# Performance work log

Hardware: AMD Instinct MI355X
Metric: run time of the kernel (lower is better)

## Reference

```python
import jax, jax.numpy as jnp
import numpy as np

N_NODES = 100000
N_EDGES = 3200000
IN_FEATS = 768
HIDDEN = 32
NUM_CLASSES = 8


def setup_inputs() -> dict:
    key = jax.random.key(0)
    ks = jax.random.split(key, 9)
    feats = jax.random.normal(ks[0], (N_NODES, IN_FEATS), dtype=jnp.float32)
    src = jax.random.randint(ks[1], (N_EDGES,), 0, N_NODES, dtype=jnp.int32)
    dst = jax.random.randint(ks[2], (N_EDGES,), 0, N_NODES, dtype=jnp.int32)
    # DGL SAGEConv params: fc_self / fc_neigh (bias=False) + separate bias
    def glorot(k, shape):
        lim = float(np.sqrt(6.0 / (shape[0] + shape[1])))
        return jax.random.uniform(k, shape, jnp.float32, -lim, lim)
    W_self1 = glorot(ks[3], (HIDDEN, IN_FEATS))
    W_neigh1 = glorot(ks[4], (HIDDEN, IN_FEATS))
    b1 = jnp.zeros((HIDDEN,), jnp.float32)
    W_self2 = glorot(ks[5], (NUM_CLASSES, HIDDEN))
    W_neigh2 = glorot(ks[6], (NUM_CLASSES, HIDDEN))
    b2 = jnp.zeros((NUM_CLASSES,), jnp.float32)
    return {"features": feats, "src": src, "dst": dst,
            "W_self1": W_self1, "W_neigh1": W_neigh1, "b1": b1,
            "W_self2": W_self2, "W_neigh2": W_neigh2, "b2": b2}


def _sage_mean_layer(x, W_self, W_neigh, b, src, dst, n_nodes):
    # DGL: lin_before_mp when in_feats > out_feats (true for both layers here)
    h = x @ W_neigh.T                      # [N, out]
    msg = h[src]                           # [E, out] gather
    agg_sum = jax.ops.segment_sum(msg, dst, num_segments=n_nodes)
    deg = jax.ops.segment_sum(jnp.ones_like(dst, dtype=x.dtype), dst,
                              num_segments=n_nodes)
    h_neigh = agg_sum / jnp.maximum(deg, 1.0)[:, None]  # zero-in-degree -> 0
    return x @ W_self.T + h_neigh + b


def reference(features, src, dst, W_self1, W_neigh1, b1, W_self2, W_neigh2, b2):
    n = features.shape[0]
    h = _sage_mean_layer(features, W_self1, W_neigh1, b1, src, dst, n)
    h = jax.nn.relu(h)
    # dropout is identity in eval mode
    out = _sage_mean_layer(h, W_self2, W_neigh2, b2, src, dst, n)
    return out
```

## Files before the change

kernel.cpp:

```cpp
#include <hip/hip_runtime.h>
#include <hip/hip_bf16.h>

#define IN_FEATS 768
#define PART_CHUNK 8192
#define SRC_BITS 17
#define SRC_MASK 0x1FFFF

typedef __attribute__((ext_vector_type(8))) short short8v;
typedef __attribute__((ext_vector_type(4))) float f32x4;

__device__ __forceinline__ unsigned short f2bf(float f) {
    union { float f; unsigned int u; } c; c.f = f;
    unsigned int r = (c.u + 0x7FFFu + ((c.u >> 16) & 1u)) >> 16;
    return (unsigned short)r;
}
__device__ __forceinline__ float bflo(unsigned int v) {
    union { unsigned int u; float f; } c; c.u = v << 16; return c.f;
}
__device__ __forceinline__ float bfhi(unsigned int v) {
    union { unsigned int u; float f; } c; c.u = v & 0xFFFF0000u; return c.f;
}
__device__ __forceinline__ short8v pack8(float4 p, float4 q) {
    short8v r;
    r[0] = (short)f2bf(p.x); r[1] = (short)f2bf(p.y);
    r[2] = (short)f2bf(p.z); r[3] = (short)f2bf(p.w);
    r[4] = (short)f2bf(q.x); r[5] = (short)f2bf(q.y);
    r[6] = (short)f2bf(q.z); r[7] = (short)f2bf(q.w);
    return r;
}

__global__ __launch_bounds__(512) void init_cursor_kernel(
    int* __restrict__ bcursor, int NB, int CAP)
{
    const int t = threadIdx.x;
    if (t < NB) bcursor[t] = t * CAP;
}

__global__ __launch_bounds__(256) void gemm_part_kernel(
    const float* __restrict__ x,
    const float* __restrict__ Wn,
    const float* __restrict__ Ws,
    const float* __restrict__ b1,
    unsigned short* __restrict__ hn1b,
    float* __restrict__ hs1,
    int N,
    const int* __restrict__ src, const int* __restrict__ dst,
    int* __restrict__ bcursor, unsigned int* __restrict__ packed,
    int NB, int E, int CAP, int nbPart)
{
    __shared__ __align__(16) unsigned char smem[36864];
    const int tid = threadIdx.x;

    if ((int)blockIdx.x < nbPart) {
        int* hcnt  = (int*)smem;
        int* hbase = hcnt + 512;

        for (int i = tid; i < NB; i += 256) hcnt[i] = 0;
        __syncthreads();

        const int start = blockIdx.x * PART_CHUNK;
        const int end   = min(start + PART_CHUNK, E);
        const int vend  = start + ((end - start) & ~3);

        for (int i = start + tid * 4; i + 3 < end; i += 1024) {
            const int4 d4 = *(const int4*)&dst[i];
            atomicAdd(&hcnt[d4.x >> 8], 1);
            atomicAdd(&hcnt[d4.y >> 8], 1);
            atomicAdd(&hcnt[d4.z >> 8], 1);
            atomicAdd(&hcnt[d4.w >> 8], 1);
        }
        for (int i = vend + tid; i < end; i += 256)
            atomicAdd(&hcnt[dst[i] >> 8], 1);
        __syncthreads();

        for (int i = tid; i < NB; i += 256) {
            const int c = hcnt[i];
            hbase[i] = c ? atomicAdd(&bcursor[i], c) : 0;
            hcnt[i] = 0;
        }
        __syncthreads();

        for (int i = start + tid * 4; i + 3 < end; i += 1024) {
            const int4 d4 = *(const int4*)&dst[i];
            const int4 s4 = *(const int4*)&src[i];
            {
                const int b = d4.x >> 8;
                const int p = hbase[b] + atomicAdd(&hcnt[b], 1);
                if (p < (b + 1) * CAP) packed[p] = ((unsigned int)(d4.x & 255) << SRC_BITS) | (unsigned int)s4.x;
            }
            {
                const int b = d4.y >> 8;
                const int p = hbase[b] + atomicAdd(&hcnt[b], 1);
                if (p < (b + 1) * CAP) packed[p] = ((unsigned int)(d4.y & 255) << SRC_BITS) | (unsigned int)s4.y;
            }
            {
                const int b = d4.z >> 8;
                const int p = hbase[b] + atomicAdd(&hcnt[b], 1);
                if (p < (b + 1) * CAP) packed[p] = ((unsigned int)(d4.z & 255) << SRC_BITS) | (unsigned int)s4.z;
            }
            {
                const int b = d4.w >> 8;
                const int p = hbase[b] + atomicAdd(&hcnt[b], 1);
                if (p < (b + 1) * CAP) packed[p] = ((unsigned int)(d4.w & 255) << SRC_BITS) | (unsigned int)s4.w;
            }
        }
        for (int i = vend + tid; i < end; i += 256) {
            const int d = dst[i];
            const int b = d >> 8;
            const int p = hbase[b] + atomicAdd(&hcnt[b], 1);
            if (p < (b + 1) * CAP) packed[p] = ((unsigned int)(d & 255) << SRC_BITS) | (unsigned int)src[i];
        }
        return;
    }

    unsigned short* AsB = (unsigned short*)smem;
    unsigned short* BsB = AsB + 2 * 64 * 72;
#define AS(b, r) (AsB + ((b) * 64 + (r)) * 72)
#define BS(b, r) (BsB + ((b) * 64 + (r)) * 72)

    const int lrow = tid >> 2;
    const int lk16 = (tid & 3) * 16;
    const int row0 = ((int)blockIdx.x - nbPart) * 64;

    const int  grow   = row0 + lrow;
    const bool rvalid = (grow < N);
    const float* xrow = x + (size_t)(rvalid ? grow : (N - 1)) * IN_FEATS;
    const float* wrow = (lrow < 32) ? (Wn + (size_t)lrow * IN_FEATS)
                                    : (Ws + (size_t)(lrow - 32) * IN_FEATS);

    const int w    = tid >> 6;
    const int l    = tid & 63;
    const int lr16 = l & 15;
    const int lk   = (l >> 4) * 8;

    f32x4 acc[4];
#pragma unroll
    for (int ct = 0; ct < 4; ++ct) acc[ct] = (f32x4){0.f, 0.f, 0.f, 0.f};

    float4 a0, a1, a2, a3, w0, w1, w2, w3;
    a0 = *(const float4*)(xrow + lk16 + 0);
    a1 = *(const float4*)(xrow + lk16 + 4);
    a2 = *(const float4*)(xrow + lk16 + 8);
    a3 = *(const float4*)(xrow + lk16 + 12);
    w0 = *(const float4*)(wrow + lk16 + 0);
    w1 = *(const float4*)(wrow + lk16 + 4);
    w2 = *(const float4*)(wrow + lk16 + 8);
    w3 = *(const float4*)(wrow + lk16 + 12);

    const int NSTEP = IN_FEATS / 64;
    for (int step = 0; step < NSTEP; ++step) {
        const int buf = step & 1;
        *(short8v*)(AS(buf, lrow) + lk16)     = pack8(a0, a1);
        *(short8v*)(AS(buf, lrow) + lk16 + 8) = pack8(a2, a3);
        *(short8v*)(BS(buf, lrow) + lk16)     = pack8(w0, w1);
        *(short8v*)(BS(buf, lrow) + lk16 + 8) = pack8(w2, w3);
        __syncthreads();

        if (step + 1 < NSTEP) {
            const int k0 = (step + 1) * 64;
            a0 = *(const float4*)(xrow + k0 + lk16 + 0);
            a1 = *(const float4*)(xrow + k0 + lk16 + 4);
            a2 = *(const float4*)(xrow + k0 + lk16 + 8);
            a3 = *(const float4*)(xrow + k0 + lk16 + 12);
            w0 = *(const float4*)(wrow + k0 + lk16 + 0);
            w1 = *(const float4*)(wrow + k0 + lk16 + 4);
            w2 = *(const float4*)(wrow + k0 + lk16 + 8);
            w3 = *(const float4*)(wrow + k0 + lk16 + 12);
        }

        short8v af0 = *(const short8v*)(AS(buf, w * 16 + lr16) + lk);
        short8v af1 = *(const short8v*)(AS(buf, w * 16 + lr16) + lk + 32);
#pragma unroll
        for (int ct = 0; ct < 4; ++ct) {
            short8v bf0 = *(const short8v*)(BS(buf, ct * 16 + lr16) + lk);
            acc[ct] = __builtin_amdgcn_mfma_f32_16x16x32_bf16(af0, bf0, acc[ct], 0, 0, 0);
        }
#pragma unroll
        for (int ct = 0; ct < 4; ++ct) {
            short8v bf1 = *(const short8v*)(BS(buf, ct * 16 + lr16) + lk + 32);
            acc[ct] = __builtin_amdgcn_mfma_f32_16x16x32_bf16(af1, bf1, acc[ct], 0, 0, 0);
        }
    }
#undef AS
#undef BS

    const int rbase = row0 + w * 16 + (l >> 4) * 4;
#pragma unroll
    for (int ct = 0; ct < 4; ++ct) {
        const int ncol = ct * 16 + lr16;
        if (ncol < 32) {
            const int half = ncol >> 4;
            const int c16  = ncol & 15;
            unsigned short* hd = hn1b + (size_t)half * N * 16;
#pragma unroll
            for (int j = 0; j < 4; ++j) {
                const int r = rbase + j;
                if (r < N) hd[(size_t)r * 16 + c16] = f2bf(acc[ct][j]);
            }
        } else {
            const int c = ncol - 32;
            const float bias = b1[c];
#pragma unroll
            for (int j = 0; j < 4; ++j) {
                const int r = rbase + j;
                if (r < N) hs1[(size_t)r * 32 + c] = acc[ct][j] + bias;
            }
        }
    }
}

__global__ __launch_bounds__(1024) void csr_finalize_kernel(
    const unsigned int* __restrict__ packed, const int* __restrict__ bcursor,
    int* __restrict__ rowstart, int* __restrict__ rowcnt,
    int* __restrict__ edge_src, int N, int CAP)
{
    __shared__ int cnt[256];
    __shared__ int sdata[256];
    __shared__ int cur[256];
    const int b = blockIdx.x;
    const int t = threadIdx.x;
    const int base = b * CAP;
    const int endp = min(bcursor[b], base + CAP);

    if (t < 256) cnt[t] = 0;
    __syncthreads();
    for (int i = base + t; i < endp; i += 1024)
        atomicAdd(&cnt[packed[i] >> SRC_BITS], 1);
    __syncthreads();

    if (t < 256) sdata[t] = cnt[t];
    __syncthreads();
    for (int off = 1; off < 256; off <<= 1) {
        const int add = (t < 256 && t >= off) ? sdata[t - off] : 0;
        __syncthreads();
        if (t < 256) sdata[t] += add;
        __syncthreads();
    }
    if (t < 256) {
        const int excl = (t > 0) ? sdata[t - 1] : 0;
        const int n = (b << 8) + t;
        if (n < N) {
            rowstart[n] = base + excl;
            rowcnt[n]   = cnt[t];
        }
        cur[t] = base + excl;
    }
    __syncthreads();

    for (int i = base + t; i < endp; i += 1024) {
        const unsigned int v = packed[i];
        const int pos = atomicAdd(&cur[v >> SRC_BITS], 1);
        edge_src[pos] = (int)(v & SRC_MASK);
    }
}

__global__ __launch_bounds__(256) void agg1_fused_kernel(
    const unsigned short* __restrict__ hn1b,
    const float* __restrict__ hs1,
    const int* __restrict__ rowstart, const int* __restrict__ rowcnt,
    const int* __restrict__ edge_src,
    const float* __restrict__ Wn2, const float* __restrict__ Ws2,
    const float* __restrict__ b2,
    unsigned short* __restrict__ hn2b, float* __restrict__ hs2, int N)
{
    __shared__ float w2[16][33];
    __shared__ float bb[8];
    __shared__ float hsm[32][33];

    const int tid = threadIdx.x;
    const int g   = tid >> 3;
    const int ln  = tid & 7;

    w2[tid >> 5][tid & 31]       = Wn2[tid];
    w2[8 + (tid >> 5)][tid & 31] = Ws2[tid];
    if (tid < 8) bb[tid] = b2[tid];

    const int n = blockIdx.x * 32 + g;
    int rs = 0, degi = 0;
    if (n < N) { rs = rowstart[n]; degi = rowcnt[n]; }
    const float inv = 1.0f / fmaxf((float)degi, 1.0f);
    const int re = rs + degi;

#pragma unroll
    for (int h = 0; h < 2; ++h) {
        const unsigned int* tab = (const unsigned int*)hn1b + (size_t)h * N * 8;
        float sx = 0.f, sy = 0.f;
        if (n < N) {
            int e = rs;
            for (; e + 4 <= re; e += 4) {
                const int s0 = edge_src[e + 0];
                const int s1 = edge_src[e + 1];
                const int s2 = edge_src[e + 2];
                const int s3 = edge_src[e + 3];
                const unsigned int v0 = tab[(size_t)s0 * 8 + ln];
                const unsigned int v1 = tab[(size_t)s1 * 8 + ln];
                const unsigned int v2 = tab[(size_t)s2 * 8 + ln];
                const unsigned int v3 = tab[(size_t)s3 * 8 + ln];
                sx += (bflo(v0) + bflo(v1)) + (bflo(v2) + bflo(v3));
                sy += (bfhi(v0) + bfhi(v1)) + (bfhi(v2) + bfhi(v3));
            }
            for (; e < re; ++e) {
                const unsigned int v = tab[(size_t)edge_src[e] * 8 + ln];
                sx += bflo(v); sy += bfhi(v);
            }
            const int f = h * 16 + 2 * ln;
            const float2 hsv = *(const float2*)(hs1 + (size_t)n * 32 + f);
            hsm[g][f + 0] = fmaxf(hsv.x + sx * inv, 0.0f);
            hsm[g][f + 1] = fmaxf(hsv.y + sy * inv, 0.0f);
        }
    }
    __syncthreads();

    if (n < N) {
        const float* hv = hsm[g];
#pragma unroll
        for (int o2 = 0; o2 < 2; ++o2) {
            const int o = o2 * 8 + ln;
            const float* wr = w2[o];
            float acc = 0.0f;
#pragma unroll
            for (int k = 0; k < 32; ++k) acc += wr[k] * hv[k];
            if (o < 8) hn2b[(size_t)n * 8 + o] = f2bf(acc);
            else       hs2[(size_t)n * 8 + (o - 8)] = acc + bb[o - 8];
        }
    }
}

__global__ __launch_bounds__(256) void agg2_fused_kernel(
    const unsigned short* __restrict__ hn2b, const float* __restrict__ hs2,
    const int* __restrict__ rowstart, const int* __restrict__ rowcnt,
    const int* __restrict__ edge_src,
    float* __restrict__ out, int N)
{
    const int tid  = threadIdx.x;
    const int g    = tid >> 4;
    const int ln   = tid & 15;
    const int slot = ln >> 2;
    const int q    = ln & 3;

    const unsigned int* hn2u = (const unsigned int*)hn2b;

    const int n = blockIdx.x * 16 + g;
    float sx = 0.f, sy = 0.f;
    int degi = 0;
    if (n < N) {
        const int rs = rowstart[n];
        degi = rowcnt[n];
        const int re = rs + degi;
        for (int e = rs + slot; e < re; e += 4) {
            const unsigned int v = hn2u[(size_t)edge_src[e] * 4 + q];
            sx += bflo(v); sy += bfhi(v);
        }
    }
    sx += __shfl_xor(sx, 4, 64);  sy += __shfl_xor(sy, 4, 64);
    sx += __shfl_xor(sx, 8, 64);  sy += __shfl_xor(sy, 8, 64);

    if (n < N && slot == 0) {
        const float inv = 1.0f / fmaxf((float)degi, 1.0f);
        const float2 s = *(const float2*)(hs2 + (size_t)n * 8 + 2 * q);
        float2 o;
        o.x = s.x + sx * inv;
        o.y = s.y + sy * inv;
        *(float2*)(out + (size_t)n * 8 + 2 * q) = o;
    }
}

extern "C" void kernel_launch(void* const* d_in, const int* in_sizes, int n_in,
                              void* d_out, int out_size, void* d_ws, size_t ws_size,
                              hipStream_t stream)
{
    const float* feats = (const float*)d_in[0];
    const int*   src   = (const int*)d_in[1];
    const int*   dst   = (const int*)d_in[2];
    const float* Ws1   = (const float*)d_in[3];
    const float* Wn1   = (const float*)d_in[4];
    const float* b1    = (const float*)d_in[5];
    const float* Ws2   = (const float*)d_in[6];
    const float* Wn2   = (const float*)d_in[7];
    const float* b2    = (const float*)d_in[8];
    float* out = (float*)d_out;

    const int N  = in_sizes[0] / IN_FEATS;
    const int E  = in_sizes[1];
    const int NB = (N + 255) >> 8;
    const int CAP = (int)((((2LL * E) / NB) + 255) & ~255LL);

    char* ws = (char*)d_ws;
    const size_t N32 = (size_t)N * 32;
    const size_t N8  = (size_t)N * 8;
    unsigned short* hn1b = (unsigned short*)ws;
    ws += ((N32 * 2 + 255) / 256) * 256;
    float* hs1 = (float*)ws;
    ws += ((N32 * 4 + 255) / 256) * 256;
    unsigned short* hn2b = (unsigned short*)ws;
    ws += ((N8 * 2 + 255) / 256) * 256;
    float* hs2 = (float*)ws;
    ws += ((N8 * 4 + 255) / 256) * 256;
    int* rowstart = (int*)ws;
    ws += (((size_t)N * 4 + 255) / 256) * 256;
    int* rowcnt = (int*)ws;
    ws += (((size_t)N * 4 + 255) / 256) * 256;
    int* bcursor = (int*)ws;
    ws += 512 * 4;
    unsigned int* packed = (unsigned int*)ws;
    ws += (((size_t)NB * CAP * 4 + 255) / 256) * 256;
    int* edge_src = (int*)ws;

    const int nbPart = (E + PART_CHUNK - 1) / PART_CHUNK;
    const int nbGemm = (N + 63) / 64;

    init_cursor_kernel<<<1, 512, 0, stream>>>(bcursor, NB, CAP);

    gemm_part_kernel<<<nbPart + nbGemm, 256, 0, stream>>>(
        feats, Wn1, Ws1, b1, hn1b, hs1, N,
        src, dst, bcursor, packed, NB, E, CAP, nbPart);

    csr_finalize_kernel<<<NB, 1024, 0, stream>>>(packed, bcursor, rowstart,
                                                 rowcnt, edge_src, N, CAP);

    agg1_fused_kernel<<<(N + 31) / 32, 256, 0, stream>>>(
        hn1b, hs1, rowstart, rowcnt, edge_src, Wn2, Ws2, b2, hn2b, hs2, N);

    agg2_fused_kernel<<<(N + 15) / 16, 256, 0, stream>>>(
        hn2b, hs2, rowstart, rowcnt, edge_src, out, N);
}
```

Baseline: 239.3 us.

## Merge all stages into one persistent cooperative kernel with grid syncs

Replaces five separate kernel launches (cursor init, partition+GEMM, CSR finalize, layer-1 aggregation, layer-2 aggregation) with a single cooperative persistent kernel that loops over work items and uses grid-wide syncs between stages. The aim is to remove launch gaps and the tail effects at kernel boundaries. In exchange the grid is capped at 4 blocks per CU times 256 CUs, which may lower occupancy for the memory-bound gather phases. The finalize stage also drops from 1024 to 256 threads per bucket, and grid.sync adds barrier overhead.

```diff
diff --git a/kernel.cpp b/kernel.cpp
--- a/kernel.cpp
+++ b/kernel.cpp
@@ -1,5 +1,8 @@
 #include <hip/hip_runtime.h>
+#include <hip/hip_cooperative_groups.h>
 #include <hip/hip_bf16.h>
+
+namespace cg = cooperative_groups;
 
 #define IN_FEATS 768
 #define PART_CHUNK 8192
@@ -29,104 +32,107 @@
     return r;
 }
 
-__global__ __launch_bounds__(512) void init_cursor_kernel(
-    int* __restrict__ bcursor, int NB, int CAP)
+struct MegaParams {
+    const float* x;
+    const float* Wn;
+    const float* Ws;
+    const float* b1;
+    const float* Wn2;
+    const float* Ws2;
+    const float* b2;
+    const int* src;
+    const int* dst;
+    unsigned short* hn1b;
+    float* hs1;
+    unsigned short* hn2b;
+    float* hs2;
+    int* rowstart;
+    int* rowcnt;
+    int* bcursor;
+    unsigned int* packed;
+    int* edge_src;
+    float* out;
+    int N, E, NB, CAP, nbPart, nbGemm;
+};
+
+__device__ __forceinline__ void partition_chunk(
+    const MegaParams& p, int chunk, int tid, unsigned char* smem)
 {
-    const int t = threadIdx.x;
-    if (t < NB) bcursor[t] = t * CAP;
-}
-
-__global__ __launch_bounds__(256) void gemm_part_kernel(
-    const float* __restrict__ x,
-    const float* __restrict__ Wn,
-    const float* __restrict__ Ws,
-    const float* __restrict__ b1,
-    unsigned short* __restrict__ hn1b,
-    float* __restrict__ hs1,
-    int N,
-    const int* __restrict__ src, const int* __restrict__ dst,
-    int* __restrict__ bcursor, unsigned int* __restrict__ packed,
-    int NB, int E, int CAP, int nbPart)
+    int* hcnt  = (int*)smem;
+    int* hbase = hcnt + 512;
+
+    for (int i = tid; i < p.NB; i += 256) hcnt[i] = 0;
+    __syncthreads();
+
+    const int start = chunk * PART_CHUNK;
+    const int end   = min(start + PART_CHUNK, p.E);
+    const int vend  = start + ((end - start) & ~3);
+
+    for (int i = start + tid * 4; i + 3 < end; i += 1024) {
+        const int4 d4 = *(const int4*)&p.dst[i];
+        atomicAdd(&hcnt[d4.x >> 8], 1);
+        atomicAdd(&hcnt[d4.y >> 8], 1);
+        atomicAdd(&hcnt[d4.z >> 8], 1);
+        atomicAdd(&hcnt[d4.w >> 8], 1);
+    }
+    for (int i = vend + tid; i < end; i += 256)
+        atomicAdd(&hcnt[p.dst[i] >> 8], 1);
+    __syncthreads();
+
+    for (int i = tid; i < p.NB; i += 256) {
+        const int c = hcnt[i];
+        hbase[i] = c ? atomicAdd(&p.bcursor[i], c) : 0;
+        hcnt[i] = 0;
+    }
+    __syncthreads();
+
+    for (int i = start + tid * 4; i + 3 < end; i += 1024) {
+        const int4 d4 = *(const int4*)&p.dst[i];
+        const int4 s4 = *(const int4*)&p.src[i];
+        {
+            const int b = d4.x >> 8;
+            const int q = hbase[b] + atomicAdd(&hcnt[b], 1);
+            if (q < (b + 1) * p.CAP) p.packed[q] = ((unsigned int)(d4.x & 255) << SRC_BITS) | (unsigned int)s4.x;
+        }
+        {
+            const int b = d4.y >> 8;
+            const int q = hbase[b] + atomicAdd(&hcnt[b], 1);
+            if (q < (b + 1) * p.CAP) p.packed[q] = ((unsigned int)(d4.y & 255) << SRC_BITS) | (unsigned int)s4.y;
+        }
+        {
+            const int b = d4.z >> 8;
+            const int q = hbase[b] + atomicAdd(&hcnt[b], 1);
+            if (q < (b + 1) * p.CAP) p.packed[q] = ((unsigned int)(d4.z & 255) << SRC_BITS) | (unsigned int)s4.z;
+        }
+        {
+            const int b = d4.w >> 8;
+            const int q = hbase[b] + atomicAdd(&hcnt[b], 1);
+            if (q < (b + 1) * p.CAP) p.packed[q] = ((unsigned int)(d4.w & 255) << SRC_BITS) | (unsigned int)s4.w;
+        }
+    }
+    for (int i = vend + tid; i < end; i += 256) {
+        const int d = p.dst[i];
+        const int b = d >> 8;
+        const int q = hbase[b] + atomicAdd(&hcnt[b], 1);
+        if (q < (b + 1) * p.CAP) p.packed[q] = ((unsigned int)(d & 255) << SRC_BITS) | (unsigned int)p.src[i];
+    }
+}
+
+__device__ __forceinline__ void gemm_tile(
+    const MegaParams& p, int t, int tid, unsigned char* smem)
 {
-    __shared__ __align__(16) unsigned char smem[36864];
-    const int tid = threadIdx.x;
-
-    if ((int)blockIdx.x < nbPart) {
-        int* hcnt  = (int*)smem;
-        int* hbase = hcnt + 512;
-
-        for (int i = tid; i < NB; i += 256) hcnt[i] = 0;
-        __syncthreads();
-
-        const int start = blockIdx.x * PART_CHUNK;
-        const int end   = min(start + PART_CHUNK, E);
-        const int vend  = start + ((end - start) & ~3);
-
-        for (int i = start + tid * 4; i + 3 < end; i += 1024) {
-            const int4 d4 = *(const int4*)&dst[i];
-            atomicAdd(&hcnt[d4.x >> 8], 1);
-            atomicAdd(&hcnt[d4.y >> 8], 1);
-            atomicAdd(&hcnt[d4.z >> 8], 1);
-            atomicAdd(&hcnt[d4.w >> 8], 1);
-        }
-        for (int i = vend + tid; i < end; i += 256)
-            atomicAdd(&hcnt[dst[i] >> 8], 1);
-        __syncthreads();
-
-        for (int i = tid; i < NB; i += 256) {
-            const int c = hcnt[i];
-            hbase[i] = c ? atomicAdd(&bcursor[i], c) : 0;
-            hcnt[i] = 0;
-        }
-        __syncthreads();
-
-        for (int i = start + tid * 4; i + 3 < end; i += 1024) {
-            const int4 d4 = *(const int4*)&dst[i];
-            const int4 s4 = *(const int4*)&src[i];
-            {
-                const int b = d4.x >> 8;
-                const int p = hbase[b] + atomicAdd(&hcnt[b], 1);
-                if (p < (b + 1) * CAP) packed[p] = ((unsigned int)(d4.x & 255) << SRC_BITS) | (unsigned int)s4.x;
-            }
-            {
-                const int b = d4.y >> 8;
-                const int p = hbase[b] + atomicAdd(&hcnt[b], 1);
-                if (p < (b + 1) * CAP) packed[p] = ((unsigned int)(d4.y & 255) << SRC_BITS) | (unsigned int)s4.y;
-            }
-            {
-                const int b = d4.z >> 8;
-                const int p = hbase[b] + atomicAdd(&hcnt[b], 1);
-                if (p < (b + 1) * CAP) packed[p] = ((unsigned int)(d4.z & 255) << SRC_BITS) | (unsigned int)s4.z;
-            }
-            {
-                const int b = d4.w >> 8;
-                const int p = hbase[b] + atomicAdd(&hcnt[b], 1);
-                if (p < (b + 1) * CAP) packed[p] = ((unsigned int)(d4.w & 255) << SRC_BITS) | (unsigned int)s4.w;
-            }
-        }
-        for (int i = vend + tid; i < end; i += 256) {
-            const int d = dst[i];
-            const int b = d >> 8;
-            const int p = hbase[b] + atomicAdd(&hcnt[b], 1);
-            if (p < (b + 1) * CAP) packed[p] = ((unsigned int)(d & 255) << SRC_BITS) | (unsigned int)src[i];
-        }
-        return;
-    }
-
     unsigned short* AsB = (unsigned short*)smem;
     unsigned short* BsB = AsB + 2 * 64 * 72;
-#define AS(b, r) (AsB + ((b) * 64 + (r)) * 72)
-#define BS(b, r) (BsB + ((b) * 64 + (r)) * 72)
 
     const int lrow = tid >> 2;
     const int lk16 = (tid & 3) * 16;
-    const int row0 = ((int)blockIdx.x - nbPart) * 64;
+    const int row0 = t * 64;
 
     const int  grow   = row0 + lrow;
-    const bool rvalid = (grow < N);
-    const float* xrow = x + (size_t)(rvalid ? grow : (N - 1)) * IN_FEATS;
-    const float* wrow = (lrow < 32) ? (Wn + (size_t)lrow * IN_FEATS)
-                                    : (Ws + (size_t)(lrow - 32) * IN_FEATS);
+    const bool rvalid = (grow < p.N);
+    const float* xrow = p.x + (size_t)(rvalid ? grow : (p.N - 1)) * IN_FEATS;
+    const float* wrow = (lrow < 32) ? (p.Wn + (size_t)lrow * IN_FEATS)
+                                    : (p.Ws + (size_t)(lrow - 32) * IN_FEATS);
 
     const int w    = tid >> 6;
     const int l    = tid & 63;
@@ -150,10 +156,12 @@
     const int NSTEP = IN_FEATS / 64;
     for (int step = 0; step < NSTEP; ++step) {
         const int buf = step & 1;
-        *(short8v*)(AS(buf, lrow) + lk16)     = pack8(a0, a1);
-        *(short8v*)(AS(buf, lrow) + lk16 + 8) = pack8(a2, a3);
-        *(short8v*)(BS(buf, lrow) + lk16)     = pack8(w0, w1);
-        *(short8v*)(BS(buf, lrow) + lk16 + 8) = pack8(w2, w3);
+        unsigned short* as = AsB + (buf * 64 + lrow) * 72;
+        unsigned short* bs = BsB + (buf * 64 + lrow) * 72;
+        *(short8v*)(as + lk16)     = pack8(a0, a1);
+        *(short8v*)(as + lk16 + 8) = pack8(a2, a3);
+        *(short8v*)(bs + lk16)     = pack8(w0, w1);
+        *(short8v*)(bs + lk16 + 8) = pack8(w2, w3);
         __syncthreads();
 
         if (step + 1 < NSTEP) {
@@ -168,21 +176,22 @@
             w3 = *(const float4*)(wrow + k0 + lk16 + 12);
         }
 
-        short8v af0 = *(const short8v*)(AS(buf, w * 16 + lr16) + lk);
-        short8v af1 = *(const short8v*)(AS(buf, w * 16 + lr16) + lk + 32);
+        const unsigned short* ar = AsB + (buf * 64 + w * 16 + lr16) * 72;
+        short8v af0 = *(const short8v*)(ar + lk);
+        short8v af1 = *(const short8v*)(ar + lk + 32);
 #pragma unroll
         for (int ct = 0; ct < 4; ++ct) {
-            short8v bf0 = *(const short8v*)(BS(buf, ct * 16 + lr16) + lk);
+            const unsigned short* br = BsB + (buf * 64 + ct * 16 + lr16) * 72;
+            short8v bf0 = *(const short8v*)(br + lk);
             acc[ct] = __builtin_amdgcn_mfma_f32_16x16x32_bf16(af0, bf0, acc[ct], 0, 0, 0);
         }
 #pragma unroll
         for (int ct = 0; ct < 4; ++ct) {
-            short8v bf1 = *(const short8v*)(BS(buf, ct * 16 + lr16) + lk + 32);
+            const unsigned short* br = BsB + (buf * 64 + ct * 16 + lr16) * 72;
+            short8v bf1 = *(const short8v*)(br + lk + 32);
             acc[ct] = __builtin_amdgcn_mfma_f32_16x16x32_bf16(af1, bf1, acc[ct], 0, 0, 0);
         }
     }
-#undef AS
-#undef BS
 
     const int rbase = row0 + w * 16 + (l >> 4) * 4;
 #pragma unroll
@@ -191,177 +200,192 @@
         if (ncol < 32) {
             const int half = ncol >> 4;
             const int c16  = ncol & 15;
-            unsigned short* hd = hn1b + (size_t)half * N * 16;
+            unsigned short* hd = p.hn1b + (size_t)half * p.N * 16;
 #pragma unroll
             for (int j = 0; j < 4; ++j) {
                 const int r = rbase + j;
-                if (r < N) hd[(size_t)r * 16 + c16] = f2bf(acc[ct][j]);
+                if (r < p.N) hd[(size_t)r * 16 + c16] = f2bf(acc[ct][j]);
             }
         } else {
             const int c = ncol - 32;
-            const float bias = b1[c];
+            const float bias = p.b1[c];
 #pragma unroll
             for (int j = 0; j < 4; ++j) {
                 const int r = rbase + j;
-                if (r < N) hs1[(size_t)r * 32 + c] = acc[ct][j] + bias;
-            }
-        }
-    }
-}
-
-__global__ __launch_bounds__(1024) void csr_finalize_kernel(
-    const unsigned int* __restrict__ packed, const int* __restrict__ bcursor,
-    int* __restrict__ rowstart, int* __restrict__ rowcnt,
-    int* __restrict__ edge_src, int N, int CAP)
+                if (r < p.N) p.hs1[(size_t)r * 32 + c] = acc[ct][j] + bias;
+            }
+        }
+    }
+}
+
+__device__ __forceinline__ void finalize_bucket(
+    const MegaParams& p, int b, int tid, unsigned char* smem)
 {
-    __shared__ int cnt[256];
-    __shared__ int sdata[256];
-    __shared__ int cur[256];
-    const int b = blockIdx.x;
-    const int t = threadIdx.x;
-    const int base = b * CAP;
-    const int endp = min(bcursor[b], base + CAP);
-
-    if (t < 256) cnt[t] = 0;
-    __syncthreads();
-    for (int i = base + t; i < endp; i += 1024)
-        atomicAdd(&cnt[packed[i] >> SRC_BITS], 1);
-    __syncthreads();
-
-    if (t < 256) sdata[t] = cnt[t];
+    int* cnt   = (int*)smem;
+    int* sdata = cnt + 256;
+    int* cur   = sdata + 256;
+
+    const int base = b * p.CAP;
+    const int endp = min(p.bcursor[b], base + p.CAP);
+
+    cnt[tid] = 0;
+    __syncthreads();
+    for (int i = base + tid; i < endp; i += 256)
+        atomicAdd(&cnt[p.packed[i] >> SRC_BITS], 1);
+    __syncthreads();
+
+    sdata[tid] = cnt[tid];
     __syncthreads();
     for (int off = 1; off < 256; off <<= 1) {
-        const int add = (t < 256 && t >= off) ? sdata[t - off] : 0;
-        __syncthreads();
-        if (t < 256) sdata[t] += add;
-        __syncthreads();
-    }
-    if (t < 256) {
-        const int excl = (t > 0) ? sdata[t - 1] : 0;
-        const int n = (b << 8) + t;
-        if (n < N) {
-            rowstart[n] = base + excl;
-            rowcnt[n]   = cnt[t];
-        }
-        cur[t] = base + excl;
-    }
-    __syncthreads();
-
-    for (int i = base + t; i < endp; i += 1024) {
-        const unsigned int v = packed[i];
+        const int add = (tid >= off) ? sdata[tid - off] : 0;
+        __syncthreads();
+        sdata[tid] += add;
+        __syncthreads();
+    }
+    const int excl = (tid > 0) ? sdata[tid - 1] : 0;
+    const int n = (b << 8) + tid;
+    if (n < p.N) {
+        p.rowstart[n] = base + excl;
+        p.rowcnt[n]   = cnt[tid];
+    }
+    cur[tid] = base + excl;
+    __syncthreads();
+
+    for (int i = base + tid; i < endp; i += 256) {
+        const unsigned int v = p.packed[i];
         const int pos = atomicAdd(&cur[v >> SRC_BITS], 1);
-        edge_src[pos] = (int)(v & SRC_MASK);
-    }
-}
-
-__global__ __launch_bounds__(256) void agg1_fused_kernel(
-    const unsigned short* __restrict__ hn1b,
-    const float* __restrict__ hs1,
-    const int* __restrict__ rowstart, const int* __restrict__ rowcnt,
-    const int* __restrict__ edge_src,
-    const float* __restrict__ Wn2, const float* __restrict__ Ws2,
-    const float* __restrict__ b2,
-    unsigned short* __restrict__ hn2b, float* __restrict__ hs2, int N)
+        p.edge_src[pos] = (int)(v & SRC_MASK);
+    }
+}
+
+__global__ __launch_bounds__(256, 4) void mega_kernel(MegaParams p)
 {
-    __shared__ float w2[16][33];
-    __shared__ float bb[8];
-    __shared__ float hsm[32][33];
-
-    const int tid = threadIdx.x;
-    const int g   = tid >> 3;
-    const int ln  = tid & 7;
-
-    w2[tid >> 5][tid & 31]       = Wn2[tid];
-    w2[8 + (tid >> 5)][tid & 31] = Ws2[tid];
-    if (tid < 8) bb[tid] = b2[tid];
-
-    const int n = blockIdx.x * 32 + g;
-    int rs = 0, degi = 0;
-    if (n < N) { rs = rowstart[n]; degi = rowcnt[n]; }
-    const float inv = 1.0f / fmaxf((float)degi, 1.0f);
-    const int re = rs + degi;
-
-#pragma unroll
-    for (int h = 0; h < 2; ++h) {
-        const unsigned int* tab = (const unsigned int*)hn1b + (size_t)h * N * 8;
-        float sx = 0.f, sy = 0.f;
-        if (n < N) {
-            int e = rs;
-            for (; e + 4 <= re; e += 4) {
-                const int s0 = edge_src[e + 0];
-                const int s1 = edge_src[e + 1];
-                const int s2 = edge_src[e + 2];
-                const int s3 = edge_src[e + 3];
-                const unsigned int v0 = tab[(size_t)s0 * 8 + ln];
-                const unsigned int v1 = tab[(size_t)s1 * 8 + ln];
-                const unsigned int v2 = tab[(size_t)s2 * 8 + ln];
-                const unsigned int v3 = tab[(size_t)s3 * 8 + ln];
-                sx += (bflo(v0) + bflo(v1)) + (bflo(v2) + bflo(v3));
-                sy += (bfhi(v0) + bfhi(v1)) + (bfhi(v2) + bfhi(v3));
-            }
-            for (; e < re; ++e) {
-                const unsigned int v = tab[(size_t)edge_src[e] * 8 + ln];
-                sx += bflo(v); sy += bfhi(v);
-            }
-            const int f = h * 16 + 2 * ln;
-            const float2 hsv = *(const float2*)(hs1 + (size_t)n * 32 + f);
-            hsm[g][f + 0] = fmaxf(hsv.x + sx * inv, 0.0f);
-            hsm[g][f + 1] = fmaxf(hsv.y + sy * inv, 0.0f);
-        }
-    }
-    __syncthreads();
-
-    if (n < N) {
-        const float* hv = hsm[g];
-#pragma unroll
-        for (int o2 = 0; o2 < 2; ++o2) {
-            const int o = o2 * 8 + ln;
-            const float* wr = w2[o];
-            float acc = 0.0f;
-#pragma unroll
-            for (int k = 0; k < 32; ++k) acc += wr[k] * hv[k];
-            if (o < 8) hn2b[(size_t)n * 8 + o] = f2bf(acc);
-            else       hs2[(size_t)n * 8 + (o - 8)] = acc + bb[o - 8];
-        }
-    }
-}
-
-__global__ __launch_bounds__(256) void agg2_fused_kernel(
-    const unsigned short* __restrict__ hn2b, const float* __restrict__ hs2,
-    const int* __restrict__ rowstart, const int* __restrict__ rowcnt,
-    const int* __restrict__ edge_src,
-    float* __restrict__ out, int N)
-{
+    __shared__ __align__(16) unsigned char smem[36864];
+    cg::grid_group gg = cg::this_grid();
     const int tid  = threadIdx.x;
-    const int g    = tid >> 4;
-    const int ln   = tid & 15;
-    const int slot = ln >> 2;
-    const int q    = ln & 3;
-
-    const unsigned int* hn2u = (const unsigned int*)hn2b;
-
-    const int n = blockIdx.x * 16 + g;
-    float sx = 0.f, sy = 0.f;
-    int degi = 0;
-    if (n < N) {
-        const int rs = rowstart[n];
-        degi = rowcnt[n];
-        const int re = rs + degi;
-        for (int e = rs + slot; e < re; e += 4) {
-            const unsigned int v = hn2u[(size_t)edge_src[e] * 4 + q];
-            sx += bflo(v); sy += bfhi(v);
-        }
-    }
-    sx += __shfl_xor(sx, 4, 64);  sy += __shfl_xor(sy, 4, 64);
-    sx += __shfl_xor(sx, 8, 64);  sy += __shfl_xor(sy, 8, 64);
-
-    if (n < N && slot == 0) {
-        const float inv = 1.0f / fmaxf((float)degi, 1.0f);
-        const float2 s = *(const float2*)(hs2 + (size_t)n * 8 + 2 * q);
-        float2 o;
-        o.x = s.x + sx * inv;
-        o.y = s.y + sy * inv;
-        *(float2*)(out + (size_t)n * 8 + 2 * q) = o;
+    const int bid  = blockIdx.x;
+    const int nblk = gridDim.x;
+
+    for (int i = bid * 256 + tid; i < p.NB; i += nblk * 256)
+        p.bcursor[i] = i * p.CAP;
+    gg.sync();
+
+    const int totalP1 = p.nbPart + p.nbGemm;
+    for (int item = bid; item < totalP1; item += nblk) {
+        if (item < p.nbPart) partition_chunk(p, item, tid, smem);
+        else                 gemm_tile(p, item - p.nbPart, tid, smem);
+        __syncthreads();
+    }
+    gg.sync();
+
+    for (int b = bid; b < p.NB; b += nblk) {
+        finalize_bucket(p, b, tid, smem);
+        __syncthreads();
+    }
+    gg.sync();
+
+    {
+        float* w2  = (float*)smem;
+        float* bb  = w2 + 16 * 33;
+        float* hsm = bb + 8;
+
+        w2[(tid >> 5) * 33 + (tid & 31)]       = p.Wn2[tid];
+        w2[(8 + (tid >> 5)) * 33 + (tid & 31)] = p.Ws2[tid];
+        if (tid < 8) bb[tid] = p.b2[tid];
+        __syncthreads();
+
+        const int g  = tid >> 3;
+        const int ln = tid & 7;
+        const int ngroups = (p.N + 31) / 32;
+
+        for (int gi = bid; gi < ngroups; gi += nblk) {
+            const int n = gi * 32 + g;
+            int rs = 0, degi = 0;
+            if (n < p.N) { rs = p.rowstart[n]; degi = p.rowcnt[n]; }
+            const float inv = 1.0f / fmaxf((float)degi, 1.0f);
+            const int re = rs + degi;
+
+#pragma unroll
+            for (int h = 0; h < 2; ++h) {
+                const unsigned int* tab = (const unsigned int*)p.hn1b + (size_t)h * p.N * 8;
+                float sx = 0.f, sy = 0.f;
+                if (n < p.N) {
+                    int e = rs;
+                    for (; e + 4 <= re; e += 4) {
+                        const int s0 = p.edge_src[e + 0];
+                        const int s1 = p.edge_src[e + 1];
+                        const int s2 = p.edge_src[e + 2];
+                        const int s3 = p.edge_src[e + 3];
+                        const unsigned int v0 = tab[(size_t)s0 * 8 + ln];
+                        const unsigned int v1 = tab[(size_t)s1 * 8 + ln];
+                        const unsigned int v2 = tab[(size_t)s2 * 8 + ln];
+                        const unsigned int v3 = tab[(size_t)s3 * 8 + ln];
+                        sx += (bflo(v0) + bflo(v1)) + (bflo(v2) + bflo(v3));
+                        sy += (bfhi(v0) + bfhi(v1)) + (bfhi(v2) + bfhi(v3));
+                    }
+                    for (; e < re; ++e) {
+                        const unsigned int v = tab[(size_t)p.edge_src[e] * 8 + ln];
+                        sx += bflo(v); sy += bfhi(v);
+                    }
+                    const int f = h * 16 + 2 * ln;
+                    const float2 hsv = *(const float2*)(p.hs1 + (size_t)n * 32 + f);
+                    hsm[g * 33 + f + 0] = fmaxf(hsv.x + sx * inv, 0.0f);
+                    hsm[g * 33 + f + 1] = fmaxf(hsv.y + sy * inv, 0.0f);
+                }
+            }
+            __syncthreads();
+
+            if (n < p.N) {
+                const float* hv = hsm + g * 33;
+#pragma unroll
+                for (int o2 = 0; o2 < 2; ++o2) {
+                    const int o = o2 * 8 + ln;
+                    const float* wr = w2 + o * 33;
+                    float acc = 0.0f;
+#pragma unroll
+                    for (int k = 0; k < 32; ++k) acc += wr[k] * hv[k];
+                    if (o < 8) p.hn2b[(size_t)n * 8 + o] = f2bf(acc);
+                    else       p.hs2[(size_t)n * 8 + (o - 8)] = acc + bb[o - 8];
+                }
+            }
+            __syncthreads();
+        }
+    }
+    gg.sync();
+
+    {
+        const int g    = tid >> 4;
+        const int ln   = tid & 15;
+        const int slot = ln >> 2;
+        const int q    = ln & 3;
+        const unsigned int* hn2u = (const unsigned int*)p.hn2b;
+        const int ng2 = (p.N + 15) / 16;
+
+        for (int gi = bid; gi < ng2; gi += nblk) {
+            const int n = gi * 16 + g;
+            float sx = 0.f, sy = 0.f;
+            int degi = 0;
+            if (n < p.N) {
+                const int rs = p.rowstart[n];
+                degi = p.rowcnt[n];
+                const int re = rs + degi;
+                for (int e = rs + slot; e < re; e += 4) {
+                    const unsigned int v = hn2u[(size_t)p.edge_src[e] * 4 + q];
+                    sx += bflo(v); sy += bfhi(v);
+                }
+            }
+            sx += __shfl_xor(sx, 4, 64);  sy += __shfl_xor(sy, 4, 64);
+            sx += __shfl_xor(sx, 8, 64);  sy += __shfl_xor(sy, 8, 64);
+
+            if (n < p.N && slot == 0) {
+                const float inv = 1.0f / fmaxf((float)degi, 1.0f);
+                const float2 s = *(const float2*)(p.hs2 + (size_t)n * 8 + 2 * q);
+                float2 o;
+                o.x = s.x + sx * inv;
+                o.y = s.y + sy * inv;
+                *(float2*)(p.out + (size_t)n * 8 + 2 * q) = o;
+            }
+        }
     }
 }
 
@@ -406,21 +430,27 @@
     ws += (((size_t)NB * CAP * 4 + 255) / 256) * 256;
     int* edge_src = (int*)ws;
 
-    const int nbPart = (E + PART_CHUNK - 1) / PART_CHUNK;
-    const int nbGemm = (N + 63) / 64;
-
-    init_cursor_kernel<<<1, 512, 0, stream>>>(bcursor, NB, CAP);
-
-    gemm_part_kernel<<<nbPart + nbGemm, 256, 0, stream>>>(
-        feats, Wn1, Ws1, b1, hn1b, hs1, N,
-        src, dst, bcursor, packed, NB, E, CAP, nbPart);
-
-    csr_finalize_kernel<<<NB, 1024, 0, stream>>>(packed, bcursor, rowstart,
-                                                 rowcnt, edge_src, N, CAP);
-
-    agg1_fused_kernel<<<(N + 31) / 32, 256, 0, stream>>>(
-        hn1b, hs1, rowstart, rowcnt, edge_src, Wn2, Ws2, b2, hn2b, hs2, N);
-
-    agg2_fused_kernel<<<(N + 15) / 16, 256, 0, stream>>>(
-        hn2b, hs2, rowstart, rowcnt, edge_src, out, N);
-}
+    MegaParams mp;
+    mp.x = feats; mp.Wn = Wn1; mp.Ws = Ws1; mp.b1 = b1;
+    mp.Wn2 = Wn2; mp.Ws2 = Ws2; mp.b2 = b2;
+    mp.src = src; mp.dst = dst;
+    mp.hn1b = hn1b; mp.hs1 = hs1; mp.hn2b = hn2b; mp.hs2 = hs2;
+    mp.rowstart = rowstart; mp.rowcnt = rowcnt;
+    mp.bcursor = bcursor; mp.packed = packed; mp.edge_src = edge_src;
+    mp.out = out;
+    mp.N = N; mp.E = E; mp.NB = NB; mp.CAP = CAP;
+    mp.nbPart = (E + PART_CHUNK - 1) / PART_CHUNK;
+    mp.nbGemm = (N + 63) / 64;
+
+    int maxPerCU = 0;
+    if (hipOccupancyMaxActiveBlocksPerMultiprocessor(&maxPerCU, mega_kernel,
+                                                     256, 0) != hipSuccess ||
+        maxPerCU < 1)
+        maxPerCU = 1;
+    if (maxPerCU > 4) maxPerCU = 4;
+    const int gridBlocks = maxPerCU * 256;
+
+    void* args[] = { (void*)&mp };
+    hipLaunchCooperativeKernel(mega_kernel, dim3(gridBlocks), dim3(256),
+                               args, 0, stream);
+}
```

Result: slower. 576.9 us (+141.0%).

## Fuse CSR finalize with layer-1 aggregation in a per-bucket kernel

Applied to the files above, without the earlier changes.

Merges the CSR finalize kernel and the first aggregation kernel into one kernel with one block per 256-node destination bucket. Each block builds its bucket's row offsets and edge_src slice, then aggregates those nodes right away, reading degree and start from shared memory. This removes a kernel launch and the global round trip for rowstart/rowcnt, and the edge_src it just wrote is likely still in cache. In exchange, the gather work now runs on only NB blocks of 1024 threads, so there is less parallelism than the old grid of N/32 blocks and occupancy may be lower.

```diff
diff --git a/kernel.cpp b/kernel.cpp
--- a/kernel.cpp
+++ b/kernel.cpp
@@ -209,21 +209,38 @@
     }
 }
 
-__global__ __launch_bounds__(1024) void csr_finalize_kernel(
+__global__ __launch_bounds__(1024) void agg1_bucket_kernel(
+    const unsigned short* __restrict__ hn1b,
+    const float* __restrict__ hs1,
     const unsigned int* __restrict__ packed, const int* __restrict__ bcursor,
     int* __restrict__ rowstart, int* __restrict__ rowcnt,
-    int* __restrict__ edge_src, int N, int CAP)
+    int* __restrict__ edge_src,
+    const float* __restrict__ Wn2, const float* __restrict__ Ws2,
+    const float* __restrict__ b2,
+    unsigned short* __restrict__ hn2b, float* __restrict__ hs2,
+    int N, int CAP)
 {
     __shared__ int cnt[256];
     __shared__ int sdata[256];
     __shared__ int cur[256];
+    __shared__ int lstart[256];
+    __shared__ float w2[16][33];
+    __shared__ float bb[8];
+    __shared__ float hsm[128][33];
+
     const int b = blockIdx.x;
     const int t = threadIdx.x;
     const int base = b * CAP;
     const int endp = min(bcursor[b], base + CAP);
 
-    if (t < 256) cnt[t] = 0;
+    if (t < 256) {
+        w2[t >> 5][t & 31]       = Wn2[t];
+        w2[8 + (t >> 5)][t & 31] = Ws2[t];
+        if (t < 8) bb[t] = b2[t];
+        cnt[t] = 0;
+    }
     __syncthreads();
+
     for (int i = base + t; i < endp; i += 1024)
         atomicAdd(&cnt[packed[i] >> SRC_BITS], 1);
     __syncthreads();
@@ -243,7 +260,8 @@
             rowstart[n] = base + excl;
             rowcnt[n]   = cnt[t];
         }
-        cur[t] = base + excl;
+        cur[t]    = base + excl;
+        lstart[t] = base + excl;
     }
     __syncthreads();
 
@@ -252,77 +270,65 @@
         const int pos = atomicAdd(&cur[v >> SRC_BITS], 1);
         edge_src[pos] = (int)(v & SRC_MASK);
     }
-}
-
-__global__ __launch_bounds__(256) void agg1_fused_kernel(
-    const unsigned short* __restrict__ hn1b,
-    const float* __restrict__ hs1,
-    const int* __restrict__ rowstart, const int* __restrict__ rowcnt,
-    const int* __restrict__ edge_src,
-    const float* __restrict__ Wn2, const float* __restrict__ Ws2,
-    const float* __restrict__ b2,
-    unsigned short* __restrict__ hn2b, float* __restrict__ hs2, int N)
-{
-    __shared__ float w2[16][33];
-    __shared__ float bb[8];
-    __shared__ float hsm[32][33];
-
-    const int tid = threadIdx.x;
-    const int g   = tid >> 3;
-    const int ln  = tid & 7;
-
-    w2[tid >> 5][tid & 31]       = Wn2[tid];
-    w2[8 + (tid >> 5)][tid & 31] = Ws2[tid];
-    if (tid < 8) bb[tid] = b2[tid];
-
-    const int n = blockIdx.x * 32 + g;
-    int rs = 0, degi = 0;
-    if (n < N) { rs = rowstart[n]; degi = rowcnt[n]; }
-    const float inv = 1.0f / fmaxf((float)degi, 1.0f);
-    const int re = rs + degi;
-
-#pragma unroll
-    for (int h = 0; h < 2; ++h) {
-        const unsigned int* tab = (const unsigned int*)hn1b + (size_t)h * N * 8;
-        float sx = 0.f, sy = 0.f;
-        if (n < N) {
-            int e = rs;
-            for (; e + 4 <= re; e += 4) {
-                const int s0 = edge_src[e + 0];
-                const int s1 = edge_src[e + 1];
-                const int s2 = edge_src[e + 2];
-                const int s3 = edge_src[e + 3];
-                const unsigned int v0 = tab[(size_t)s0 * 8 + ln];
-                const unsigned int v1 = tab[(size_t)s1 * 8 + ln];
-                const unsigned int v2 = tab[(size_t)s2 * 8 + ln];
-                const unsigned int v3 = tab[(size_t)s3 * 8 + ln];
-                sx += (bflo(v0) + bflo(v1)) + (bflo(v2) + bflo(v3));
-                sy += (bfhi(v0) + bfhi(v1)) + (bfhi(v2) + bfhi(v3));
-            }
-            for (; e < re; ++e) {
-                const unsigned int v = tab[(size_t)edge_src[e] * 8 + ln];
-                sx += bflo(v); sy += bfhi(v);
-            }
-            const int f = h * 16 + 2 * ln;
-            const float2 hsv = *(const float2*)(hs1 + (size_t)n * 32 + f);
-            hsm[g][f + 0] = fmaxf(hsv.x + sx * inv, 0.0f);
-            hsm[g][f + 1] = fmaxf(hsv.y + sy * inv, 0.0f);
-        }
-    }
     __syncthreads();
 
-    if (n < N) {
-        const float* hv = hsm[g];
-#pragma unroll
-        for (int o2 = 0; o2 < 2; ++o2) {
-            const int o = o2 * 8 + ln;
-            const float* wr = w2[o];
-            float acc = 0.0f;
-#pragma unroll
-            for (int k = 0; k < 32; ++k) acc += wr[k] * hv[k];
-            if (o < 8) hn2b[(size_t)n * 8 + o] = f2bf(acc);
-            else       hs2[(size_t)n * 8 + (o - 8)] = acc + bb[o - 8];
-        }
+    const int g  = t >> 3;
+    const int ln = t & 7;
+    const unsigned int* hn1u = (const unsigned int*)hn1b;
+
+    for (int r = 0; r < 2; ++r) {
+        const int nl = r * 128 + g;
+        const int n  = (b << 8) + nl;
+        const bool ok = (n < N);
+        int rs = 0, degi = 0;
+        if (ok) { rs = lstart[nl]; degi = cnt[nl]; }
+        const float inv = 1.0f / fmaxf((float)degi, 1.0f);
+        const int re = rs + degi;
+
+#pragma unroll
+        for (int h = 0; h < 2; ++h) {
+            const unsigned int* tab = hn1u + (size_t)h * N * 8;
+            float sx = 0.f, sy = 0.f;
+            if (ok) {
+                int e = rs;
+                for (; e + 4 <= re; e += 4) {
+                    const int s0 = edge_src[e + 0];
+                    const int s1 = edge_src[e + 1];
+                    const int s2 = edge_src[e + 2];
+                    const int s3 = edge_src[e + 3];
+                    const unsigned int v0 = tab[(size_t)s0 * 8 + ln];
+                    const unsigned int v1 = tab[(size_t)s1 * 8 + ln];
+                    const unsigned int v2 = tab[(size_t)s2 * 8 + ln];
+                    const unsigned int v3 = tab[(size_t)s3 * 8 + ln];
+                    sx += (bflo(v0) + bflo(v1)) + (bflo(v2) + bflo(v3));
+                    sy += (bfhi(v0) + bfhi(v1)) + (bfhi(v2) + bfhi(v3));
+                }
+                for (; e < re; ++e) {
+                    const unsigned int v = tab[(size_t)edge_src[e] * 8 + ln];
+                    sx += bflo(v); sy += bfhi(v);
+                }
+                const int f = h * 16 + 2 * ln;
+                const float2 hsv = *(const float2*)(hs1 + (size_t)n * 32 + f);
+                hsm[g][f + 0] = fmaxf(hsv.x + sx * inv, 0.0f);
+                hsm[g][f + 1] = fmaxf(hsv.y + sy * inv, 0.0f);
+            }
+        }
+        __syncthreads();
+
+        if (ok) {
+            const float* hv = hsm[g];
+#pragma unroll
+            for (int o2 = 0; o2 < 2; ++o2) {
+                const int o = o2 * 8 + ln;
+                const float* wr = w2[o];
+                float acc = 0.0f;
+#pragma unroll
+                for (int k = 0; k < 32; ++k) acc += wr[k] * hv[k];
+                if (o < 8) hn2b[(size_t)n * 8 + o] = f2bf(acc);
+                else       hs2[(size_t)n * 8 + (o - 8)] = acc + bb[o - 8];
+            }
+        }
+        __syncthreads();
     }
 }
 
@@ -415,11 +421,9 @@
         feats, Wn1, Ws1, b1, hn1b, hs1, N,
         src, dst, bcursor, packed, NB, E, CAP, nbPart);
 
-    csr_finalize_kernel<<<NB, 1024, 0, stream>>>(packed, bcursor, rowstart,
-                                                 rowcnt, edge_src, N, CAP);
-
-    agg1_fused_kernel<<<(N + 31) / 32, 256, 0, stream>>>(
-        hn1b, hs1, rowstart, rowcnt, edge_src, Wn2, Ws2, b2, hn2b, hs2, N);
+    agg1_bucket_kernel<<<NB, 1024, 0, stream>>>(
+        hn1b, hs1, packed, bcursor, rowstart, rowcnt, edge_src,
+        Wn2, Ws2, b2, hn2b, hs2, N, CAP);
 
     agg2_fused_kernel<<<(N + 15) / 16, 256, 0, stream>>>(
         hn2b, hs2, rowstart, rowcnt, edge_src, out, N);
```

Result: slower. 254.8 us (+6.4%).

## Replace global atomic bucket cursors with fixed per-chunk cells in edge partitioning

Applied to the files above, without the earlier changes.

Edge partitioning now writes each chunk's edges for a destination bucket into a fixed-size slot of CELL entries, and records per-chunk counts in a matrix. This removes the global atomicAdd on bucket cursors and the separate init_cursor kernel launch. The finalize kernel scans every cell of a bucket and masks by the recorded counts, then places CSR rows at fixed ECAP strides. In exchange the finalize pass reads more padded slots and does an integer divide per slot. A cell or bucket that exceeds its capacity would silently drop or overrun edges on skewed graphs.

```diff
diff --git a/kernel.cpp b/kernel.cpp
--- a/kernel.cpp
+++ b/kernel.cpp
@@ -5,6 +5,8 @@
 #define PART_CHUNK 8192
 #define SRC_BITS 17
 #define SRC_MASK 0x1FFFF
+#define CELL 56
+#define ECAP 10240
 
 typedef __attribute__((ext_vector_type(8))) short short8v;
 typedef __attribute__((ext_vector_type(4))) float f32x4;
@@ -27,13 +29,6 @@
     r[4] = (short)f2bf(q.x); r[5] = (short)f2bf(q.y);
     r[6] = (short)f2bf(q.z); r[7] = (short)f2bf(q.w);
     return r;
-}
-
-__global__ __launch_bounds__(512) void init_cursor_kernel(
-    int* __restrict__ bcursor, int NB, int CAP)
-{
-    const int t = threadIdx.x;
-    if (t < NB) bcursor[t] = t * CAP;
 }
 
 __global__ __launch_bounds__(256) void gemm_part_kernel(
@@ -45,20 +40,21 @@
     float* __restrict__ hs1,
     int N,
     const int* __restrict__ src, const int* __restrict__ dst,
-    int* __restrict__ bcursor, unsigned int* __restrict__ packed,
-    int NB, int E, int CAP, int nbPart)
+    unsigned int* __restrict__ packed,
+    int* __restrict__ cntm,
+    int NB, int E, int nbPart)
 {
     __shared__ __align__(16) unsigned char smem[36864];
     const int tid = threadIdx.x;
 
     if ((int)blockIdx.x < nbPart) {
-        int* hcnt  = (int*)smem;
-        int* hbase = hcnt + 512;
-
-        for (int i = tid; i < NB; i += 256) hcnt[i] = 0;
-        __syncthreads();
-
-        const int start = blockIdx.x * PART_CHUNK;
+        int* hcnt = (int*)smem;
+        const int c = blockIdx.x;
+
+        for (int i = tid; i < 512; i += 256) hcnt[i] = 0;
+        __syncthreads();
+
+        const int start = c * PART_CHUNK;
         const int end   = min(start + PART_CHUNK, E);
         const int vend  = start + ((end - start) & ~3);
 
@@ -74,8 +70,7 @@
         __syncthreads();
 
         for (int i = tid; i < NB; i += 256) {
-            const int c = hcnt[i];
-            hbase[i] = c ? atomicAdd(&bcursor[i], c) : 0;
+            cntm[c * 512 + i] = min(hcnt[i], CELL);
             hcnt[i] = 0;
         }
         __syncthreads();
@@ -85,30 +80,35 @@
             const int4 s4 = *(const int4*)&src[i];
             {
                 const int b = d4.x >> 8;
-                const int p = hbase[b] + atomicAdd(&hcnt[b], 1);
-                if (p < (b + 1) * CAP) packed[p] = ((unsigned int)(d4.x & 255) << SRC_BITS) | (unsigned int)s4.x;
+                const int j = atomicAdd(&hcnt[b], 1);
+                if (j < CELL) packed[((size_t)b * nbPart + c) * CELL + j] =
+                    ((unsigned int)(d4.x & 255) << SRC_BITS) | (unsigned int)s4.x;
             }
             {
                 const int b = d4.y >> 8;
-                const int p = hbase[b] + atomicAdd(&hcnt[b], 1);
-                if (p < (b + 1) * CAP) packed[p] = ((unsigned int)(d4.y & 255) << SRC_BITS) | (unsigned int)s4.y;
+                const int j = atomicAdd(&hcnt[b], 1);
+                if (j < CELL) packed[((size_t)b * nbPart + c) * CELL + j] =
+                    ((unsigned int)(d4.y & 255) << SRC_BITS) | (unsigned int)s4.y;
             }
             {
                 const int b = d4.z >> 8;
-                const int p = hbase[b] + atomicAdd(&hcnt[b], 1);
-                if (p < (b + 1) * CAP) packed[p] = ((unsigned int)(d4.z & 255) << SRC_BITS) | (unsigned int)s4.z;
+                const int j = atomicAdd(&hcnt[b], 1);
+                if (j < CELL) packed[((size_t)b * nbPart + c) * CELL + j] =
+                    ((unsigned int)(d4.z & 255) << SRC_BITS) | (unsigned int)s4.z;
             }
             {
                 const int b = d4.w >> 8;
-                const int p = hbase[b] + atomicAdd(&hcnt[b], 1);
-                if (p < (b + 1) * CAP) packed[p] = ((unsigned int)(d4.w & 255) << SRC_BITS) | (unsigned int)s4.w;
+                const int j = atomicAdd(&hcnt[b], 1);
+                if (j < CELL) packed[((size_t)b * nbPart + c) * CELL + j] =
+                    ((unsigned int)(d4.w & 255) << SRC_BITS) | (unsigned int)s4.w;
             }
         }
         for (int i = vend + tid; i < end; i += 256) {
             const int d = dst[i];
             const int b = d >> 8;
-            const int p = hbase[b] + atomicAdd(&hcnt[b], 1);
-            if (p < (b + 1) * CAP) packed[p] = ((unsigned int)(d & 255) << SRC_BITS) | (unsigned int)src[i];
+            const int j = atomicAdd(&hcnt[b], 1);
+            if (j < CELL) packed[((size_t)b * nbPart + c) * CELL + j] =
+                ((unsigned int)(d & 255) << SRC_BITS) | (unsigned int)src[i];
         }
         return;
     }
@@ -210,22 +210,29 @@
 }
 
 __global__ __launch_bounds__(1024) void csr_finalize_kernel(
-    const unsigned int* __restrict__ packed, const int* __restrict__ bcursor,
+    const unsigned int* __restrict__ packed, const int* __restrict__ cntm,
     int* __restrict__ rowstart, int* __restrict__ rowcnt,
-    int* __restrict__ edge_src, int N, int CAP)
+    int* __restrict__ edge_src, int N, int NB, int nbPart)
 {
+    __shared__ int cellcnt[512];
     __shared__ int cnt[256];
     __shared__ int sdata[256];
     __shared__ int cur[256];
     const int b = blockIdx.x;
     const int t = threadIdx.x;
-    const int base = b * CAP;
-    const int endp = min(bcursor[b], base + CAP);
-
+    const int S = nbPart * CELL;
+    const size_t base_in = (size_t)b * S;
+
+    for (int c = t; c < nbPart; c += 1024) cellcnt[c] = cntm[c * 512 + b];
     if (t < 256) cnt[t] = 0;
     __syncthreads();
-    for (int i = base + t; i < endp; i += 1024)
-        atomicAdd(&cnt[packed[i] >> SRC_BITS], 1);
+
+    for (int i = t; i < S; i += 1024) {
+        const int c = i / CELL;
+        const int j = i - c * CELL;
+        if (j < cellcnt[c])
+            atomicAdd(&cnt[packed[base_in + i] >> SRC_BITS], 1);
+    }
     __syncthreads();
 
     if (t < 256) sdata[t] = cnt[t];
@@ -240,17 +247,21 @@
         const int excl = (t > 0) ? sdata[t - 1] : 0;
         const int n = (b << 8) + t;
         if (n < N) {
-            rowstart[n] = base + excl;
+            rowstart[n] = b * ECAP + excl;
             rowcnt[n]   = cnt[t];
         }
-        cur[t] = base + excl;
+        cur[t] = b * ECAP + excl;
     }
     __syncthreads();
 
-    for (int i = base + t; i < endp; i += 1024) {
-        const unsigned int v = packed[i];
-        const int pos = atomicAdd(&cur[v >> SRC_BITS], 1);
-        edge_src[pos] = (int)(v & SRC_MASK);
+    for (int i = t; i < S; i += 1024) {
+        const int c = i / CELL;
+        const int j = i - c * CELL;
+        if (j < cellcnt[c]) {
+            const unsigned int v = packed[base_in + i];
+            const int pos = atomicAdd(&cur[v >> SRC_BITS], 1);
+            edge_src[pos] = (int)(v & SRC_MASK);
+        }
     }
 }
 
@@ -383,7 +394,8 @@
     const int N  = in_sizes[0] / IN_FEATS;
     const int E  = in_sizes[1];
     const int NB = (N + 255) >> 8;
-    const int CAP = (int)((((2LL * E) / NB) + 255) & ~255LL);
+    const int nbPart = (E + PART_CHUNK - 1) / PART_CHUNK;
+    const int nbGemm = (N + 63) / 64;
 
     char* ws = (char*)d_ws;
     const size_t N32 = (size_t)N * 32;
@@ -400,23 +412,18 @@
     ws += (((size_t)N * 4 + 255) / 256) * 256;
     int* rowcnt = (int*)ws;
     ws += (((size_t)N * 4 + 255) / 256) * 256;
-    int* bcursor = (int*)ws;
-    ws += 512 * 4;
+    int* cntm = (int*)ws;
+    ws += (((size_t)nbPart * 512 * 4 + 255) / 256) * 256;
     unsigned int* packed = (unsigned int*)ws;
-    ws += (((size_t)NB * CAP * 4 + 255) / 256) * 256;
+    ws += (((size_t)NB * nbPart * CELL * 4 + 255) / 256) * 256;
     int* edge_src = (int*)ws;
-
-    const int nbPart = (E + PART_CHUNK - 1) / PART_CHUNK;
-    const int nbGemm = (N + 63) / 64;
-
-    init_cursor_kernel<<<1, 512, 0, stream>>>(bcursor, NB, CAP);
 
     gemm_part_kernel<<<nbPart + nbGemm, 256, 0, stream>>>(
         feats, Wn1, Ws1, b1, hn1b, hs1, N,
-        src, dst, bcursor, packed, NB, E, CAP, nbPart);
-
-    csr_finalize_kernel<<<NB, 1024, 0, stream>>>(packed, bcursor, rowstart,
-                                                 rowcnt, edge_src, N, CAP);
+        src, dst, packed, cntm, NB, E, nbPart);
+
+    csr_finalize_kernel<<<NB, 1024, 0, stream>>>(packed, cntm, rowstart,
+                                                 rowcnt, edge_src, N, NB, nbPart);
 
     agg1_fused_kernel<<<(N + 31) / 32, 256, 0, stream>>>(
         hn1b, hs1, rowstart, rowcnt, edge_src, Wn2, Ws2, b2, hn2b, hs2, N);
```

After: 243.3 us. Within noise of the previous version (+1.7%).
